# Kernel tuning notes

Measured on AMD Instinct MI355X. Metric: run time of the kernel, lower is better.

Reference implementation:

```python
import jax, jax.numpy as jnp
import numpy as np

N_NODES = 50000
N_EDGES = 800000
IN_CH = 128
HID = 64
N_LAYERS = 14
EPS_MSG = 1e-7
EPS_SM = 1e-16
LN_EPS = 1e-5


def setup_inputs() -> dict:
    key = jax.random.key(0)
    ks = jax.random.split(key, 8)
    x = jax.random.normal(ks[0], (N_NODES, IN_CH), dtype=jnp.float32)
    edge_index = jax.random.randint(ks[1], (2, N_EDGES), 0, N_NODES, dtype=jnp.int64)
    enc_W = jax.random.normal(ks[2], (IN_CH, HID), dtype=jnp.float32) / np.sqrt(IN_CH)
    enc_b = jnp.zeros((HID,), dtype=jnp.float32)
    mlp_W = jax.random.normal(ks[3], (N_LAYERS, HID, HID), dtype=jnp.float32) / np.sqrt(HID)
    mlp_b = jnp.zeros((N_LAYERS, HID), dtype=jnp.float32)
    t = jnp.ones((N_LAYERS,), dtype=jnp.float32)  # learn_t, init t=1.0
    return {"x": x, "edge_index": edge_index, "enc_W": enc_W, "enc_b": enc_b,
            "mlp_W": mlp_W, "mlp_b": mlp_b, "t": t}


def _layernorm(h):
    # LayerNorm(elementwise_affine=False) over last dim
    mu = jnp.mean(h, axis=-1, keepdims=True)
    var = jnp.mean((h - mu) ** 2, axis=-1, keepdims=True)
    return (h - mu) * jax.lax.rsqrt(var + LN_EPS)


def _segment_softmax(scores, seg, num_segments):
    # per-target-node, per-channel softmax over incoming edges
    m = jax.ops.segment_max(scores, seg, num_segments=num_segments)
    e = jnp.exp(scores - m[seg])
    s = jax.ops.segment_sum(e, seg, num_segments=num_segments)
    return e / (s[seg] + EPS_SM)


def _genconv(h, src, dst, W, b, t):
    # GENConv: msg = relu(x_j) + eps; softmax_sg aggregation (weights detached);
    # out = MLP(aggr + x) where MLP is a single Linear
    msg = jax.nn.relu(h[src]) + EPS_MSG                       # [E, H]
    alpha = _segment_softmax(t * msg, dst, N_NODES)           # [E, H]
    alpha = jax.lax.stop_gradient(alpha)                      # 'softmax_sg'
    aggr = jax.ops.segment_sum(msg * alpha, dst, num_segments=N_NODES)
    return (aggr + h) @ W + b


def reference(x, edge_index, enc_W, enc_b, mlp_W, mlp_b, t):
    src, dst = edge_index[0], edge_index[1]
    h = x @ enc_W + enc_b                                     # node encoder
    h = _genconv(h, src, dst, mlp_W[0], mlp_b[0], t[0])       # layers[0].conv

    def body(carry, params):
        W, b, tt = params
        y = jax.nn.relu(_layernorm(carry))                    # res+ pre-norm/act
        y = _genconv(y, src, dst, W, b, tt)                   # dropout inactive (eval)
        return carry + y, None

    h, _ = jax.lax.scan(body, h, (mlp_W[1:], mlp_b[1:], t[1:]))
    h = jax.nn.relu(_layernorm(h))                            # final norm + act
    return jax.nn.log_softmax(h, axis=-1)
```

## Files before the change

kernel.cpp:

```cpp
#include <hip/hip_runtime.h>

#define NN 50000
#define NE 800000
#define INC 128
#define HIDC 64
#define NL 14
#define EPS_MSG 1e-7f
#define EPS_SM 1e-16f
#define LN_EPS 1e-5f
#define LOG2E 1.44269504088896f

#define SCAN_B 256
#define NB_SCAN ((NN + SCAN_B - 1) / SCAN_B)

__device__ __forceinline__ float wave_sum(float v) {
    #pragma unroll
    for (int o = 32; o > 0; o >>= 1) v += __shfl_xor(v, o, 64);
    return v;
}
__device__ __forceinline__ float wave_max(float v) {
    #pragma unroll
    for (int o = 32; o > 0; o >>= 1) v = fmaxf(v, __shfl_xor(v, o, 64));
    return v;
}
__device__ __forceinline__ float bcast(float x, int l) {
    return __int_as_float(__builtin_amdgcn_readlane(__float_as_int(x), l));
}
__device__ __forceinline__ float fexp2(float x) {
    float r; asm("v_exp_f32 %0, %1" : "=v"(r) : "v"(x)); return r;
}
__device__ __forceinline__ unsigned pack_bf2(float lo, float hi) {
    unsigned ul = __float_as_uint(lo); ul += 0x7fffu + ((ul >> 16) & 1u);
    unsigned uh = __float_as_uint(hi); uh += 0x7fffu + ((uh >> 16) & 1u);
    return (ul >> 16) | (uh & 0xffff0000u);
}

__global__ void k_hist(const int* __restrict__ dst, int* __restrict__ deg) {
    int i = blockIdx.x * blockDim.x + threadIdx.x;
    if (i < NE) atomicAdd(&deg[dst[i]], 1);
}

__global__ void k_part(const int* __restrict__ deg, int* __restrict__ part) {
    __shared__ int sm[SCAN_B];
    int b = blockIdx.x;
    int i = b * SCAN_B + threadIdx.x;
    sm[threadIdx.x] = (i < NN) ? deg[i] : 0;
    __syncthreads();
    for (int s = SCAN_B / 2; s > 0; s >>= 1) {
        if (threadIdx.x < s) sm[threadIdx.x] += sm[threadIdx.x + s];
        __syncthreads();
    }
    if (threadIdx.x == 0) part[b] = sm[0];
}

__global__ void k_scanpart(const int* __restrict__ part, int* __restrict__ partOfs) {
    __shared__ int sm[SCAN_B];
    int t = threadIdx.x;
    int own = (t < NB_SCAN) ? part[t] : 0;
    sm[t] = own;
    __syncthreads();
    for (int o = 1; o < SCAN_B; o <<= 1) {
        int v = (t >= o) ? sm[t - o] : 0;
        __syncthreads();
        sm[t] += v;
        __syncthreads();
    }
    if (t < NB_SCAN) partOfs[t] = sm[t] - own;
}

__global__ void k_scanfinal(const int* __restrict__ deg, const int* __restrict__ partOfs,
                            int* __restrict__ rowOfs, int* __restrict__ rowCur) {
    __shared__ int sm[SCAN_B];
    int b = blockIdx.x, t = threadIdx.x;
    int i = b * SCAN_B + t;
    int d = (i < NN) ? deg[i] : 0;
    sm[t] = d;
    __syncthreads();
    for (int o = 1; o < SCAN_B; o <<= 1) {
        int v = (t >= o) ? sm[t - o] : 0;
        __syncthreads();
        sm[t] += v;
        __syncthreads();
    }
    if (i < NN) {
        int r = partOfs[b] + sm[t] - d;
        rowOfs[i] = r;
        rowCur[i] = r;
    }
    if (i == 0) rowOfs[NN] = NE;
}

__global__ void k_scatter(const int* __restrict__ src, const int* __restrict__ dst,
                          int* __restrict__ rowCur, unsigned short* __restrict__ csrU) {
    int i = blockIdx.x * blockDim.x + threadIdx.x;
    if (i < NE) {
        int p = atomicAdd(&rowCur[dst[i]], 1);
        csrU[p] = (unsigned short)src[i];
    }
}

__global__ __launch_bounds__(256) void k_enc(const float* __restrict__ x,
                                             const float* __restrict__ W,
                                             const float* __restrict__ bias,
                                             const float* __restrict__ tptr,
                                             float* __restrict__ h,
                                             unsigned* __restrict__ B0) {
    __shared__ float XL[32 * INC];
    __shared__ float WL[INC * HIDC];
    int tid = threadIdx.x;
    for (int i = tid; i < (INC * HIDC) / 4; i += 256)
        ((float4*)WL)[i] = ((const float4*)W)[i];
    int r0 = blockIdx.x * 32;
    for (int i = tid; i < (32 * INC) / 4; i += 256) {
        int row = i >> 5;
        float4 val = make_float4(0.f, 0.f, 0.f, 0.f);
        if (r0 + row < NN) val = ((const float4*)x)[(size_t)(r0 + row) * 32 + (i & 31)];
        ((float4*)XL)[i] = val;
    }
    __syncthreads();
    int lane = tid & 63, w = tid >> 6;
    int pl = lane >> 5, wd = (lane & 31) >> 1;
    float bv = bias[lane];
    float sc = tptr[0] * LOG2E;
    #pragma unroll
    for (int i = 0; i < 4; i++) {
        int ra = w * 8 + i * 2, rb = ra + 1;
        float a0 = 0.f, a1 = 0.f, a2 = 0.f, a3 = 0.f;
        float c0 = 0.f, c1 = 0.f, c2 = 0.f, c3 = 0.f;
        #pragma unroll
        for (int k = 0; k < INC; k += 4) {
            float4 xa = *(const float4*)&XL[ra * INC + k];
            float4 xb = *(const float4*)&XL[rb * INC + k];
            float w0 = WL[(k + 0) * HIDC + lane];
            float w1 = WL[(k + 1) * HIDC + lane];
            float w2 = WL[(k + 2) * HIDC + lane];
            float w3 = WL[(k + 3) * HIDC + lane];
            a0 = fmaf(xa.x, w0, a0); a1 = fmaf(xa.y, w1, a1);
            a2 = fmaf(xa.z, w2, a2); a3 = fmaf(xa.w, w3, a3);
            c0 = fmaf(xb.x, w0, c0); c1 = fmaf(xb.y, w1, c1);
            c2 = fmaf(xb.z, w2, c2); c3 = fmaf(xb.w, w3, c3);
        }
        int ga = r0 + ra, gb = r0 + rb;
        float va = bv + ((a0 + a1) + (a2 + a3));
        float vb = bv + ((c0 + c1) + (c2 + c3));
        float sa = sc * fmaxf(va, 0.f), sb = sc * fmaxf(vb, 0.f);
        float pa = __shfl_xor(sa, 1, 64);
        float pb = __shfl_xor(sb, 1, 64);
        if (ga < NN) {
            h[(size_t)ga * HIDC + lane] = va;
            if (!(lane & 1)) B0[((size_t)pl * NN + ga) * 16 + wd] = pack_bf2(sa, pa);
        }
        if (gb < NN) {
            h[(size_t)gb * HIDC + lane] = vb;
            if (!(lane & 1)) B0[((size_t)pl * NN + gb) * 16 + wd] = pack_bf2(sb, pb);
        }
    }
}

template<bool FIRST>
__global__ __launch_bounds__(256) void k_aggr(const float* __restrict__ henc,
                                              const unsigned* __restrict__ Bin,
                                              const int* __restrict__ rowOfs,
                                              const unsigned short* __restrict__ csrU,
                                              const float* __restrict__ tptr,
                                              float* __restrict__ A) {
    int lane = threadIdx.x & 63;
    int wid = (blockIdx.x * 256 + threadIdx.x) >> 6;
    int p = (wid >= NN) ? 1 : 0;
    int v = wid - p * NN;
    int g = lane >> 3;
    int c = lane & 7;
    const char* basec = (const char*)Bin + (((size_t)p * NN) << 6) + (c << 3);
    float invs = 1.0f / (tptr[0] * LOG2E);

    int e0 = rowOfs[v], e1 = rowOfs[v + 1];
    float se0 = 0.f, se1 = 0.f, se2 = 0.f, se3 = 0.f;
    float sw0 = 0.f, sw1 = 0.f, sw2 = 0.f, sw3 = 0.f;
    int e = e0;
    for (; e + 16 <= e1; e += 16) {
        #pragma unroll
        for (int j = 0; j < 2; j++) {
            int off = (int)csrU[e + 8 * j + g] << 6;
            uint2 q = *(const uint2*)(basec + off);
            float g0 = __uint_as_float(q.x << 16);
            float g1 = __uint_as_float(q.x & 0xffff0000u);
            float g2 = __uint_as_float(q.y << 16);
            float g3 = __uint_as_float(q.y & 0xffff0000u);
            float w0 = fexp2(g0), w1 = fexp2(g1), w2 = fexp2(g2), w3 = fexp2(g3);
            se0 += w0; sw0 = fmaf(g0, w0, sw0);
            se1 += w1; sw1 = fmaf(g1, w1, sw1);
            se2 += w2; sw2 = fmaf(g2, w2, sw2);
            se3 += w3; sw3 = fmaf(g3, w3, sw3);
        }
    }
    if (e < e1) {
        #pragma unroll
        for (int j = 0; j < 2; j++) {
            int ee = e + 8 * j + g;
            bool valid = ee < e1;
            int off = (int)csrU[valid ? ee : e0] << 6;
            uint2 q = *(const uint2*)(basec + off);
            float g0 = __uint_as_float(q.x << 16);
            float g1 = __uint_as_float(q.x & 0xffff0000u);
            float g2 = __uint_as_float(q.y << 16);
            float g3 = __uint_as_float(q.y & 0xffff0000u);
            float w0 = valid ? fexp2(g0) : 0.f;
            float w1 = valid ? fexp2(g1) : 0.f;
            float w2 = valid ? fexp2(g2) : 0.f;
            float w3 = valid ? fexp2(g3) : 0.f;
            se0 += w0; sw0 = fmaf(g0, w0, sw0);
            se1 += w1; sw1 = fmaf(g1, w1, sw1);
            se2 += w2; sw2 = fmaf(g2, w2, sw2);
            se3 += w3; sw3 = fmaf(g3, w3, sw3);
        }
    }
    #pragma unroll
    for (int m = 8; m <= 32; m <<= 1) {
        se0 += __shfl_xor(se0, m, 64); sw0 += __shfl_xor(sw0, m, 64);
        se1 += __shfl_xor(se1, m, 64); sw1 += __shfl_xor(sw1, m, 64);
        se2 += __shfl_xor(se2, m, 64); sw2 += __shfl_xor(sw2, m, 64);
        se3 += __shfl_xor(se3, m, 64); sw3 += __shfl_xor(sw3, m, 64);
    }
    if (g == 0) {
        float4 r;
        r.x = sw0 / (se0 + EPS_SM) * invs + EPS_MSG;
        r.y = sw1 / (se1 + EPS_SM) * invs + EPS_MSG;
        r.z = sw2 / (se2 + EPS_SM) * invs + EPS_MSG;
        r.w = sw3 / (se3 + EPS_SM) * invs + EPS_MSG;
        if (FIRST) {
            float4 s4 = ((const float4*)henc)[(size_t)v * 16 + p * 8 + c];
            r.x += s4.x; r.y += s4.y; r.z += s4.z; r.w += s4.w;
        }
        ((float4*)A)[(size_t)v * 16 + p * 8 + c] = r;
    }
}

template<bool LNRES, int MODE>
__global__ __launch_bounds__(256) void k_mlp(const float* __restrict__ A,
                                             float* __restrict__ h,
                                             unsigned* __restrict__ Bout,
                                             const float* __restrict__ W,
                                             const float* __restrict__ b,
                                             const float* __restrict__ tnext) {
    __shared__ float WL[HIDC * HIDC];
    for (int i = threadIdx.x; i < (HIDC * HIDC) / 4; i += 256)
        ((float4*)WL)[i] = ((const float4*)W)[i];
    __syncthreads();

    int lane = threadIdx.x & 63;
    int wid = (blockIdx.x * 256 + threadIdx.x) >> 6;
    int nw = (gridDim.x * 256) >> 6;
    int pl = lane >> 5, wd = (lane & 31) >> 1;
    float bv = b[lane];
    float sc = (MODE == 0) ? tnext[0] * LOG2E : 0.f;

    for (int v = wid; v < NN; v += nw) {
        float a = A[(size_t)v * HIDC + lane];
        float base = bv;
        if (LNRES) {
            float hv = h[(size_t)v * HIDC + lane];
            float mu = wave_sum(hv) * (1.f / 64.f);
            float d = hv - mu;
            float var = wave_sum(d * d) * (1.f / 64.f);
            a += fmaxf(d * rsqrtf(var + LN_EPS), 0.f);
            base += hv;
        }
        float a0 = 0.f, a1 = 0.f, a2 = 0.f, a3 = 0.f;
        #pragma unroll
        for (int k = 0; k < 64; k += 4) {
            a0 = fmaf(bcast(a, k + 0), WL[(k + 0) * HIDC + lane], a0);
            a1 = fmaf(bcast(a, k + 1), WL[(k + 1) * HIDC + lane], a1);
            a2 = fmaf(bcast(a, k + 2), WL[(k + 2) * HIDC + lane], a2);
            a3 = fmaf(bcast(a, k + 3), WL[(k + 3) * HIDC + lane], a3);
        }
        float acc = base + ((a0 + a1) + (a2 + a3));

        if (MODE == 1) {
            float mu = wave_sum(acc) * (1.f / 64.f);
            float d = acc - mu;
            float var = wave_sum(d * d) * (1.f / 64.f);
            float z = fmaxf(d * rsqrtf(var + LN_EPS), 0.f);
            float m = wave_max(z);
            float s2 = wave_sum(fexp2((z - m) * LOG2E));
            h[(size_t)v * HIDC + lane] = z - (m + __logf(s2));
        } else {
            h[(size_t)v * HIDC + lane] = acc;
            float mu = wave_sum(acc) * (1.f / 64.f);
            float d = acc - mu;
            float var = wave_sum(d * d) * (1.f / 64.f);
            float y = sc * fmaxf(d * rsqrtf(var + LN_EPS), 0.f);
            float yp = __shfl_xor(y, 1, 64);
            if (!(lane & 1)) Bout[((size_t)pl * NN + v) * 16 + wd] = pack_bf2(y, yp);
        }
    }
}

extern "C" void kernel_launch(void* const* d_in, const int* in_sizes, int n_in,
                              void* d_out, int out_size, void* d_ws, size_t ws_size,
                              hipStream_t stream) {
    const float* x    = (const float*)d_in[0];
    const int*   ei   = (const int*)d_in[1];
    const float* encW = (const float*)d_in[2];
    const float* encb = (const float*)d_in[3];
    const float* mlpW = (const float*)d_in[4];
    const float* mlpb = (const float*)d_in[5];
    const float* t    = (const float*)d_in[6];

    float* h = (float*)d_out;

    char* ws = (char*)d_ws;
    size_t off = 0;
    auto alloc = [&](size_t bytes) -> void* {
        void* p = ws + off;
        off += (bytes + 255) / 256 * 256;
        return p;
    };
    float*          henc   = (float*)alloc((size_t)NN * HIDC * 4);
    float*          A      = (float*)alloc((size_t)NN * HIDC * 4);
    unsigned*       B0     = (unsigned*)alloc((size_t)NN * 32 * 4);
    unsigned*       B1     = (unsigned*)alloc((size_t)NN * 32 * 4);
    int*            deg    = (int*)alloc((size_t)NN * 4);
    int*            rowOfs = (int*)alloc((size_t)(NN + 1) * 4);
    int*            rowCur = (int*)alloc((size_t)NN * 4);
    int*            part   = (int*)alloc((size_t)NB_SCAN * 4);
    int*            partOf = (int*)alloc((size_t)NB_SCAN * 4);
    unsigned short* csrU   = (unsigned short*)alloc((size_t)NE * 2);

    const int* src = ei;
    const int* dst = ei + NE;

    hipMemsetAsync(deg, 0, (size_t)NN * 4, stream);

    k_hist<<<(NE + 255) / 256, 256, 0, stream>>>(dst, deg);
    k_part<<<NB_SCAN, SCAN_B, 0, stream>>>(deg, part);
    k_scanpart<<<1, SCAN_B, 0, stream>>>(part, partOf);
    k_scanfinal<<<NB_SCAN, SCAN_B, 0, stream>>>(deg, partOf, rowOfs, rowCur);
    k_scatter<<<(NE + 255) / 256, 256, 0, stream>>>(src, dst, rowCur, csrU);

    k_enc<<<(NN + 31) / 32, 256, 0, stream>>>(x, encW, encb, t, henc, B0);

    k_aggr<true><<<25000, 256, 0, stream>>>(henc, B0, rowOfs, csrU, t, A);
    k_mlp<false, 0><<<2048, 256, 0, stream>>>(A, h, B1, mlpW, mlpb, t + 1);

    for (int l = 1; l < NL - 1; l++) {
        unsigned* Bi = (l & 1) ? B1 : B0;
        unsigned* Bo = (l & 1) ? B0 : B1;
        k_aggr<false><<<25000, 256, 0, stream>>>(nullptr, Bi, rowOfs, csrU, t + l, A);
        k_mlp<true, 0><<<2048, 256, 0, stream>>>(A, h, Bo,
                                                 mlpW + (size_t)l * HIDC * HIDC,
                                                 mlpb + (size_t)l * HIDC, t + l + 1);
    }
    k_aggr<false><<<25000, 256, 0, stream>>>(nullptr, B1, rowOfs, csrU, t + (NL - 1), A);
    k_mlp<true, 1><<<2048, 256, 0, stream>>>(A, h, nullptr,
                                             mlpW + (size_t)(NL - 1) * HIDC * HIDC,
                                             mlpb + (size_t)(NL - 1) * HIDC, nullptr);
}
```

Measured before the change: 1.133 ms.

## Precompute exp and g*exp per node in fp16 instead of per-edge exp

The producer kernels now compute exp2(g) and g*exp2(g) once per node and store both as packed fp16, so the aggregation kernel only gathers and sums and no longer evaluates an exponential per edge. The gather buffer is re-laid out into 4 channel partitions with a zeroed pad row, which lets tail edges index a dummy row instead of taking a masked path. The aggregation grid becomes 2D, with each lane loading a uint4 and 16 edges processed per iteration. Gather bytes per edge double, and fp16 storage of exp values risks overflow or precision loss, since no max subtraction is done.

```diff
diff --git a/kernel.cpp b/kernel.cpp
--- a/kernel.cpp
+++ b/kernel.cpp
@@ -1,4 +1,5 @@
 #include <hip/hip_runtime.h>
+#include <hip/hip_fp16.h>
 
 #define NN 50000
 #define NE 800000
@@ -9,7 +10,7 @@
 #define EPS_SM 1e-16f
 #define LN_EPS 1e-5f
 #define LOG2E 1.44269504088896f
-
+#define NROW (NN + 1)
 #define SCAN_B 256
 #define NB_SCAN ((NN + SCAN_B - 1) / SCAN_B)
 
@@ -29,10 +30,9 @@
 __device__ __forceinline__ float fexp2(float x) {
     float r; asm("v_exp_f32 %0, %1" : "=v"(r) : "v"(x)); return r;
 }
-__device__ __forceinline__ unsigned pack_bf2(float lo, float hi) {
-    unsigned ul = __float_as_uint(lo); ul += 0x7fffu + ((ul >> 16) & 1u);
-    unsigned uh = __float_as_uint(hi); uh += 0x7fffu + ((uh >> 16) & 1u);
-    return (ul >> 16) | (uh & 0xffff0000u);
+__device__ __forceinline__ unsigned pk_f16(float lo, float hi) {
+    unsigned r; asm("v_cvt_pkrtz_f16_f32 %0, %1, %2" : "=v"(r) : "v"(lo), "v"(hi));
+    return r;
 }
 
 __global__ void k_hist(const int* __restrict__ dst, int* __restrict__ deg) {
@@ -96,6 +96,29 @@
     if (i < NE) {
         int p = atomicAdd(&rowCur[dst[i]], 1);
         csrU[p] = (unsigned short)src[i];
+    }
+}
+
+__global__ void k_zpad(unsigned* __restrict__ B0, unsigned* __restrict__ B1) {
+    int i = threadIdx.x;
+    unsigned* B = (i < 64) ? B0 : B1;
+    int j = i & 63;
+    int p = j >> 4, w = j & 15;
+    B[((size_t)p * NROW + NN) * 16 + w] = 0;
+}
+
+__device__ __forceinline__ void write_ep(unsigned* __restrict__ B, int v, int lane,
+                                         float y, float sc) {
+    float G = sc * y;
+    float E = fexp2(G);
+    float P = G * E;
+    float Ep = __shfl_xor(E, 1, 64);
+    float Pp = __shfl_xor(P, 1, 64);
+    if (!(lane & 1)) {
+        unsigned we = pk_f16(E, Ep);
+        unsigned wp = pk_f16(P, Pp);
+        int p = lane >> 4, k = (lane & 15) >> 1;
+        ((uint2*)B)[((size_t)p * NROW + v) * 8 + k] = make_uint2(we, wp);
     }
 }
 
@@ -119,7 +142,6 @@
     }
     __syncthreads();
     int lane = tid & 63, w = tid >> 6;
-    int pl = lane >> 5, wd = (lane & 31) >> 1;
     float bv = bias[lane];
     float sc = tptr[0] * LOG2E;
     #pragma unroll
@@ -143,16 +165,13 @@
         int ga = r0 + ra, gb = r0 + rb;
         float va = bv + ((a0 + a1) + (a2 + a3));
         float vb = bv + ((c0 + c1) + (c2 + c3));
-        float sa = sc * fmaxf(va, 0.f), sb = sc * fmaxf(vb, 0.f);
-        float pa = __shfl_xor(sa, 1, 64);
-        float pb = __shfl_xor(sb, 1, 64);
         if (ga < NN) {
             h[(size_t)ga * HIDC + lane] = va;
-            if (!(lane & 1)) B0[((size_t)pl * NN + ga) * 16 + wd] = pack_bf2(sa, pa);
+            write_ep(B0, ga, lane, fmaxf(va, 0.f), sc);
         }
         if (gb < NN) {
             h[(size_t)gb * HIDC + lane] = vb;
-            if (!(lane & 1)) B0[((size_t)pl * NN + gb) * 16 + wd] = pack_bf2(sb, pb);
+            write_ep(B0, gb, lane, fmaxf(vb, 0.f), sc);
         }
     }
 }
@@ -165,73 +184,47 @@
                                               const float* __restrict__ tptr,
                                               float* __restrict__ A) {
     int lane = threadIdx.x & 63;
-    int wid = (blockIdx.x * 256 + threadIdx.x) >> 6;
-    int p = (wid >= NN) ? 1 : 0;
-    int v = wid - p * NN;
-    int g = lane >> 3;
-    int c = lane & 7;
-    const char* basec = (const char*)Bin + (((size_t)p * NN) << 6) + (c << 3);
+    int v = blockIdx.x * 4 + (threadIdx.x >> 6);
+    int p = blockIdx.y;
+    int eg = lane >> 2;
+    int q = lane & 3;
+    const uint4* base = (const uint4*)(Bin + (size_t)p * NROW * 16);
     float invs = 1.0f / (tptr[0] * LOG2E);
 
     int e0 = rowOfs[v], e1 = rowOfs[v + 1];
     float se0 = 0.f, se1 = 0.f, se2 = 0.f, se3 = 0.f;
     float sw0 = 0.f, sw1 = 0.f, sw2 = 0.f, sw3 = 0.f;
-    int e = e0;
-    for (; e + 16 <= e1; e += 16) {
-        #pragma unroll
-        for (int j = 0; j < 2; j++) {
-            int off = (int)csrU[e + 8 * j + g] << 6;
-            uint2 q = *(const uint2*)(basec + off);
-            float g0 = __uint_as_float(q.x << 16);
-            float g1 = __uint_as_float(q.x & 0xffff0000u);
-            float g2 = __uint_as_float(q.y << 16);
-            float g3 = __uint_as_float(q.y & 0xffff0000u);
-            float w0 = fexp2(g0), w1 = fexp2(g1), w2 = fexp2(g2), w3 = fexp2(g3);
-            se0 += w0; sw0 = fmaf(g0, w0, sw0);
-            se1 += w1; sw1 = fmaf(g1, w1, sw1);
-            se2 += w2; sw2 = fmaf(g2, w2, sw2);
-            se3 += w3; sw3 = fmaf(g3, w3, sw3);
-        }
-    }
-    if (e < e1) {
-        #pragma unroll
-        for (int j = 0; j < 2; j++) {
-            int ee = e + 8 * j + g;
-            bool valid = ee < e1;
-            int off = (int)csrU[valid ? ee : e0] << 6;
-            uint2 q = *(const uint2*)(basec + off);
-            float g0 = __uint_as_float(q.x << 16);
-            float g1 = __uint_as_float(q.x & 0xffff0000u);
-            float g2 = __uint_as_float(q.y << 16);
-            float g3 = __uint_as_float(q.y & 0xffff0000u);
-            float w0 = valid ? fexp2(g0) : 0.f;
-            float w1 = valid ? fexp2(g1) : 0.f;
-            float w2 = valid ? fexp2(g2) : 0.f;
-            float w3 = valid ? fexp2(g3) : 0.f;
-            se0 += w0; sw0 = fmaf(g0, w0, sw0);
-            se1 += w1; sw1 = fmaf(g1, w1, sw1);
-            se2 += w2; sw2 = fmaf(g2, w2, sw2);
-            se3 += w3; sw3 = fmaf(g3, w3, sw3);
-        }
+    for (int e = e0; e < e1; e += 16) {
+        int ee = e + eg;
+        int idx = (ee < e1) ? (int)__builtin_nontemporal_load(csrU + ee) : NN;
+        uint4 qd = base[(size_t)idx * 4 + q];
+        __half2 E01 = *reinterpret_cast<__half2*>(&qd.x);
+        __half2 P01 = *reinterpret_cast<__half2*>(&qd.y);
+        __half2 E23 = *reinterpret_cast<__half2*>(&qd.z);
+        __half2 P23 = *reinterpret_cast<__half2*>(&qd.w);
+        se0 += __low2float(E01); se1 += __high2float(E01);
+        sw0 += __low2float(P01); sw1 += __high2float(P01);
+        se2 += __low2float(E23); se3 += __high2float(E23);
+        sw2 += __low2float(P23); sw3 += __high2float(P23);
     }
     #pragma unroll
-    for (int m = 8; m <= 32; m <<= 1) {
+    for (int m = 4; m <= 32; m <<= 1) {
         se0 += __shfl_xor(se0, m, 64); sw0 += __shfl_xor(sw0, m, 64);
         se1 += __shfl_xor(se1, m, 64); sw1 += __shfl_xor(sw1, m, 64);
         se2 += __shfl_xor(se2, m, 64); sw2 += __shfl_xor(sw2, m, 64);
         se3 += __shfl_xor(se3, m, 64); sw3 += __shfl_xor(sw3, m, 64);
     }
-    if (g == 0) {
+    if (lane < 4) {
         float4 r;
         r.x = sw0 / (se0 + EPS_SM) * invs + EPS_MSG;
         r.y = sw1 / (se1 + EPS_SM) * invs + EPS_MSG;
         r.z = sw2 / (se2 + EPS_SM) * invs + EPS_MSG;
         r.w = sw3 / (se3 + EPS_SM) * invs + EPS_MSG;
         if (FIRST) {
-            float4 s4 = ((const float4*)henc)[(size_t)v * 16 + p * 8 + c];
+            float4 s4 = ((const float4*)henc)[(size_t)v * 16 + p * 4 + lane];
             r.x += s4.x; r.y += s4.y; r.z += s4.z; r.w += s4.w;
         }
-        ((float4*)A)[(size_t)v * 16 + p * 8 + c] = r;
+        ((float4*)A)[(size_t)v * 16 + p * 4 + lane] = r;
     }
 }
 
@@ -250,7 +243,6 @@
     int lane = threadIdx.x & 63;
     int wid = (blockIdx.x * 256 + threadIdx.x) >> 6;
     int nw = (gridDim.x * 256) >> 6;
-    int pl = lane >> 5, wd = (lane & 31) >> 1;
     float bv = b[lane];
     float sc = (MODE == 0) ? tnext[0] * LOG2E : 0.f;
 
@@ -288,9 +280,8 @@
             float mu = wave_sum(acc) * (1.f / 64.f);
             float d = acc - mu;
             float var = wave_sum(d * d) * (1.f / 64.f);
-            float y = sc * fmaxf(d * rsqrtf(var + LN_EPS), 0.f);
-            float yp = __shfl_xor(y, 1, 64);
-            if (!(lane & 1)) Bout[((size_t)pl * NN + v) * 16 + wd] = pack_bf2(y, yp);
+            float y = fmaxf(d * rsqrtf(var + LN_EPS), 0.f);
+            write_ep(Bout, v, lane, y, sc);
         }
     }
 }
@@ -317,8 +308,8 @@
     };
     float*          henc   = (float*)alloc((size_t)NN * HIDC * 4);
     float*          A      = (float*)alloc((size_t)NN * HIDC * 4);
-    unsigned*       B0     = (unsigned*)alloc((size_t)NN * 32 * 4);
-    unsigned*       B1     = (unsigned*)alloc((size_t)NN * 32 * 4);
+    unsigned*       B0     = (unsigned*)alloc((size_t)4 * NROW * 16 * 4);
+    unsigned*       B1     = (unsigned*)alloc((size_t)4 * NROW * 16 * 4);
     int*            deg    = (int*)alloc((size_t)NN * 4);
     int*            rowOfs = (int*)alloc((size_t)(NN + 1) * 4);
     int*            rowCur = (int*)alloc((size_t)NN * 4);
@@ -336,21 +327,23 @@
     k_scanpart<<<1, SCAN_B, 0, stream>>>(part, partOf);
     k_scanfinal<<<NB_SCAN, SCAN_B, 0, stream>>>(deg, partOf, rowOfs, rowCur);
     k_scatter<<<(NE + 255) / 256, 256, 0, stream>>>(src, dst, rowCur, csrU);
+    k_zpad<<<1, 128, 0, stream>>>(B0, B1);
 
     k_enc<<<(NN + 31) / 32, 256, 0, stream>>>(x, encW, encb, t, henc, B0);
 
-    k_aggr<true><<<25000, 256, 0, stream>>>(henc, B0, rowOfs, csrU, t, A);
+    dim3 agrid(12500, 4);
+    k_aggr<true><<<agrid, 256, 0, stream>>>(henc, B0, rowOfs, csrU, t, A);
     k_mlp<false, 0><<<2048, 256, 0, stream>>>(A, h, B1, mlpW, mlpb, t + 1);
 
     for (int l = 1; l < NL - 1; l++) {
         unsigned* Bi = (l & 1) ? B1 : B0;
         unsigned* Bo = (l & 1) ? B0 : B1;
-        k_aggr<false><<<25000, 256, 0, stream>>>(nullptr, Bi, rowOfs, csrU, t + l, A);
+        k_aggr<false><<<agrid, 256, 0, stream>>>(nullptr, Bi, rowOfs, csrU, t + l, A);
         k_mlp<true, 0><<<2048, 256, 0, stream>>>(A, h, Bo,
                                                  mlpW + (size_t)l * HIDC * HIDC,
                                                  mlpb + (size_t)l * HIDC, t + l + 1);
     }
-    k_aggr<false><<<25000, 256, 0, stream>>>(nullptr, B1, rowOfs, csrU, t + (NL - 1), A);
+    k_aggr<false><<<agrid, 256, 0, stream>>>(nullptr, B1, rowOfs, csrU, t + (NL - 1), A);
     k_mlp<true, 1><<<2048, 256, 0, stream>>>(A, h, nullptr,
                                              mlpW + (size_t)(NL - 1) * HIDC * HIDC,
                                              mlpb + (size_t)(NL - 1) * HIDC, nullptr);
```

Measured after the change: 1.674 ms. 47.8% more time.

## Partition CSR scatter by destination range and make encoder a persistent wave-per-node kernel

Applied to the files above, without the earlier changes.

The scatter kernel now splits destination nodes into 8 ranges, and each block group handles only edges whose target falls in its range. Atomics on rowCur then cluster in a smaller address window, which should improve cache locality, at the cost of each group reading the full edge list. The encoder is rewritten as a grid-stride, wave-per-node kernel that loads the weight matrix into shared memory once per block. It broadcasts input values with readlane instead of staging x tiles in LDS, which cuts LDS traffic and block count but drops the two-row register reuse of weights.

```diff
diff --git a/kernel.cpp b/kernel.cpp
--- a/kernel.cpp
+++ b/kernel.cpp
@@ -9,7 +9,7 @@
 #define EPS_SM 1e-16f
 #define LN_EPS 1e-5f
 #define LOG2E 1.44269504088896f
-
+#define DPX 6250
 #define SCAN_B 256
 #define NB_SCAN ((NN + SCAN_B - 1) / SCAN_B)
 
@@ -92,10 +92,16 @@
 
 __global__ void k_scatter(const int* __restrict__ src, const int* __restrict__ dst,
                           int* __restrict__ rowCur, unsigned short* __restrict__ csrU) {
-    int i = blockIdx.x * blockDim.x + threadIdx.x;
-    if (i < NE) {
-        int p = atomicAdd(&rowCur[dst[i]], 1);
-        csrU[p] = (unsigned short)src[i];
+    int k = blockIdx.x & 7;
+    int bi = blockIdx.x >> 3;
+    int nb = gridDim.x >> 3;
+    int lo = k * DPX;
+    for (int i = bi * 256 + threadIdx.x; i < NE; i += nb * 256) {
+        int d = dst[i];
+        if ((unsigned)(d - lo) < (unsigned)DPX) {
+            int p = atomicAdd(&rowCur[d], 1);
+            csrU[p] = (unsigned short)src[i];
+        }
     }
 }
 
@@ -105,55 +111,31 @@
                                              const float* __restrict__ tptr,
                                              float* __restrict__ h,
                                              unsigned* __restrict__ B0) {
-    __shared__ float XL[32 * INC];
     __shared__ float WL[INC * HIDC];
-    int tid = threadIdx.x;
-    for (int i = tid; i < (INC * HIDC) / 4; i += 256)
+    for (int i = threadIdx.x; i < (INC * HIDC) / 4; i += 256)
         ((float4*)WL)[i] = ((const float4*)W)[i];
-    int r0 = blockIdx.x * 32;
-    for (int i = tid; i < (32 * INC) / 4; i += 256) {
-        int row = i >> 5;
-        float4 val = make_float4(0.f, 0.f, 0.f, 0.f);
-        if (r0 + row < NN) val = ((const float4*)x)[(size_t)(r0 + row) * 32 + (i & 31)];
-        ((float4*)XL)[i] = val;
-    }
-    __syncthreads();
-    int lane = tid & 63, w = tid >> 6;
+    __syncthreads();
+    int lane = threadIdx.x & 63;
+    int wid = (blockIdx.x * 256 + threadIdx.x) >> 6;
+    int nw = (gridDim.x * 256) >> 6;
     int pl = lane >> 5, wd = (lane & 31) >> 1;
     float bv = bias[lane];
     float sc = tptr[0] * LOG2E;
-    #pragma unroll
-    for (int i = 0; i < 4; i++) {
-        int ra = w * 8 + i * 2, rb = ra + 1;
+    for (int v = wid; v < NN; v += nw) {
+        float2 xv = ((const float2*)x)[(size_t)v * 64 + lane];
         float a0 = 0.f, a1 = 0.f, a2 = 0.f, a3 = 0.f;
-        float c0 = 0.f, c1 = 0.f, c2 = 0.f, c3 = 0.f;
         #pragma unroll
         for (int k = 0; k < INC; k += 4) {
-            float4 xa = *(const float4*)&XL[ra * INC + k];
-            float4 xb = *(const float4*)&XL[rb * INC + k];
-            float w0 = WL[(k + 0) * HIDC + lane];
-            float w1 = WL[(k + 1) * HIDC + lane];
-            float w2 = WL[(k + 2) * HIDC + lane];
-            float w3 = WL[(k + 3) * HIDC + lane];
-            a0 = fmaf(xa.x, w0, a0); a1 = fmaf(xa.y, w1, a1);
-            a2 = fmaf(xa.z, w2, a2); a3 = fmaf(xa.w, w3, a3);
-            c0 = fmaf(xb.x, w0, c0); c1 = fmaf(xb.y, w1, c1);
-            c2 = fmaf(xb.z, w2, c2); c3 = fmaf(xb.w, w3, c3);
-        }
-        int ga = r0 + ra, gb = r0 + rb;
+            a0 = fmaf(bcast(xv.x, k >> 1),       WL[(k + 0) * HIDC + lane], a0);
+            a1 = fmaf(bcast(xv.y, k >> 1),       WL[(k + 1) * HIDC + lane], a1);
+            a2 = fmaf(bcast(xv.x, (k >> 1) + 1), WL[(k + 2) * HIDC + lane], a2);
+            a3 = fmaf(bcast(xv.y, (k >> 1) + 1), WL[(k + 3) * HIDC + lane], a3);
+        }
         float va = bv + ((a0 + a1) + (a2 + a3));
-        float vb = bv + ((c0 + c1) + (c2 + c3));
-        float sa = sc * fmaxf(va, 0.f), sb = sc * fmaxf(vb, 0.f);
+        h[(size_t)v * HIDC + lane] = va;
+        float sa = sc * fmaxf(va, 0.f);
         float pa = __shfl_xor(sa, 1, 64);
-        float pb = __shfl_xor(sb, 1, 64);
-        if (ga < NN) {
-            h[(size_t)ga * HIDC + lane] = va;
-            if (!(lane & 1)) B0[((size_t)pl * NN + ga) * 16 + wd] = pack_bf2(sa, pa);
-        }
-        if (gb < NN) {
-            h[(size_t)gb * HIDC + lane] = vb;
-            if (!(lane & 1)) B0[((size_t)pl * NN + gb) * 16 + wd] = pack_bf2(sb, pb);
-        }
+        if (!(lane & 1)) B0[((size_t)pl * NN + v) * 16 + wd] = pack_bf2(sa, pa);
     }
 }
 
@@ -335,9 +317,9 @@
     k_part<<<NB_SCAN, SCAN_B, 0, stream>>>(deg, part);
     k_scanpart<<<1, SCAN_B, 0, stream>>>(part, partOf);
     k_scanfinal<<<NB_SCAN, SCAN_B, 0, stream>>>(deg, partOf, rowOfs, rowCur);
-    k_scatter<<<(NE + 255) / 256, 256, 0, stream>>>(src, dst, rowCur, csrU);
-
-    k_enc<<<(NN + 31) / 32, 256, 0, stream>>>(x, encW, encb, t, henc, B0);
+    k_scatter<<<2048, 256, 0, stream>>>(src, dst, rowCur, csrU);
+
+    k_enc<<<1280, 256, 0, stream>>>(x, encW, encb, t, henc, B0);
 
     k_aggr<true><<<25000, 256, 0, stream>>>(henc, B0, rowOfs, csrU, t, A);
     k_mlp<false, 0><<<2048, 256, 0, stream>>>(A, h, B1, mlpW, mlpb, t + 1);
```

Measured after the change: 1.136 ms. No clear change (+0.3%).
